# Optimization experiments

Measured on AMD Instinct MI355X. Metric: run time of the kernel, lower is better.

Reference implementation:

```python
import jax, jax.numpy as jnp
import numpy as np

EPS = 1e-4  # IRLS smoothing epsilon

def _corr(x, k):
    # x: [C,H,W], k: [kh,kw]; cross-correlation, 'same' output, replicate (clamp) boundary
    ph, pw = k.shape[0] // 2, k.shape[1] // 2
    xp = jnp.pad(x, ((0, 0), (ph, ph), (pw, pw)), mode='edge')
    out = jax.lax.conv_general_dilated(xp[:, None], k[None, None].astype(x.dtype), (1, 1), 'VALID', dimension_numbers=('NCHW', 'OIHW', 'NCHW'))
    return out[:, 0]

def _flip(k):
    return k[::-1, ::-1]

def _forward(blurred, kernel, reg_kernels, reg_kernel_weights, reg_target_kernels, reg_powers, num_irls_iter, num_cg_iter):
    n = reg_kernels.shape[0]
    w_kernel = jnp.ones_like(blurred)                       # data-term weights (ones, as in forward)
    w_reg = jnp.ones((n,) + blurred.shape, blurred.dtype)   # IRLS reg weights, start at 1
    lam = reg_kernel_weights ** 2                           # squared weights keep A PSD

    def R(x, ks):  # apply each reg kernel -> [N,C,H,W]
        return jax.vmap(lambda k: _corr(x, k))(ks)

    def RT(y, ks):  # adjoint: correlate with flipped kernels, y: [N,C,H,W]
        return jax.vmap(lambda yi, k: _corr(yi, _flip(k)))(y, ks)

    def A(x, w_reg):  # A = K^T W K + sum_n lam_n R_n^T W_n R_n
        data = _corr(w_kernel * _corr(x, kernel), _flip(kernel))
        reg = jnp.einsum('n,nchw->chw', lam, RT(w_reg * R(x, reg_kernels), reg_kernels))
        return data + reg

    Tb = R(blurred, reg_target_kernels)           # regularization targets T_n b
    KtWb = _corr(w_kernel * blurred, _flip(kernel))
    x0 = blurred
    for _ in range(num_irls_iter):
        # DeconvCGInit: rhs and initial residual/search direction
        rhs = KtWb + jnp.einsum('n,nchw->chw', lam, RT(w_reg * Tb, reg_kernels))
        x = x0
        r = rhs - A(x, w_reg)
        p = r
        # DeconvCGIter: standard CG updates
        for _ in range(num_cg_iter):
            Ap = A(p, w_reg)
            rr = jnp.sum(r * r)
            alpha = rr / jnp.sum(p * Ap)
            x = x + alpha * p
            r = r - alpha * Ap
            beta = jnp.sum(r * r) / rr
            p = r + beta * p
        x0 = x
        # DeconvCGWeight: IRLS reweighting w_n = p_n * (|R_n x - T_n b| + eps)^(p_n - 2)
        d = R(x0, reg_kernels) - Tb
        pw = reg_powers[:, None, None, None]
        w_reg = pw * jnp.power(jnp.abs(d) + EPS, pw - 2.0)
    return x0

def setup_inputs():
    key = jax.random.key(0)
    ks = jax.random.split(key, 6)
    C, H, W = 3, 1024, 1024
    NREG, RKS, BKS = 5, 5, 15
    blurred = jax.random.uniform(ks[0], (C, H, W), jnp.float32)
    kernel = jax.random.uniform(ks[1], (BKS, BKS), jnp.float32)
    kernel = kernel / jnp.sum(kernel)  # normalized blur kernel
    rk = 0.1 * jax.random.normal(ks[2], (NREG, RKS, RKS), jnp.float32)
    rk = rk.at[0, 2, 2].add(-2.0).at[0, 3, 2].add(1.0).at[0, 2, 3].add(1.0)  # gradient stencil init
    rkw = 0.1 * jax.random.normal(ks[3], (NREG,), jnp.float32)
    rkw = rkw.at[0].add(1.0)
    rtk = 0.1 * jax.random.normal(ks[4], (NREG, RKS, RKS), jnp.float32)
    rp = 1.0 + 0.02 * jax.random.normal(ks[5], (NREG,), jnp.float32)
    return {"blurred": blurred, "kernel": kernel, "reg_kernels": rk, "reg_kernel_weights": rkw, "reg_target_kernels": rtk, "reg_powers": rp, "num_irls_iter": 2, "num_cg_iter": 4}

def reference(blurred, kernel, reg_kernels, reg_kernel_weights, reg_target_kernels, reg_powers, num_irls_iter, num_cg_iter):
    return _forward(blurred, kernel, reg_kernels, reg_kernel_weights, reg_target_kernels, reg_powers, num_irls_iter, num_cg_iter)
```

## Files before the change

kernel.cpp:

```cpp
#include <hip/hip_runtime.h>
#include <math.h>

#define HH 1024
#define WW 1024
#define CHN 3
#define PLANE (HH*WW)
#define IMG (CHN*PLANE)
#define NREG 5
#define EPSV 1e-4f

#define OFF_WREG 0
#define OFF_KTWB (5*IMG)
#define OFF_T    (6*IMG)
#define OFF_R    (7*IMG)
#define OFF_P    (8*IMG)
#define OFF_AP   (9*IMG)
#define OFF_PART (10*IMG)
#define OFF_SCAL (10*IMG + 3072)

__global__ __launch_bounds__(256) void k_init(const float4* __restrict__ b,
                                              float4* __restrict__ x,
                                              float4* __restrict__ wreg) {
  const int stride = gridDim.x * 256;
  const float4 one = make_float4(1.f, 1.f, 1.f, 1.f);
  for (int i = blockIdx.x * 256 + threadIdx.x; i < NREG * IMG / 4; i += stride) {
    wreg[i] = one;
    if (i < IMG / 4) x[i] = b[i];
  }
}

template <bool FLIP>
__global__ __launch_bounds__(256) void k_corr15(const float* __restrict__ in,
                                                const float* __restrict__ k15,
                                                float* __restrict__ out) {
  __shared__ float tile[142 * 78];
  const int c = blockIdx.z;
  const int R0 = blockIdx.y * 128;
  const int C0 = blockIdx.x * 64;
  const float* inc = in + c * PLANE;
  for (int i = threadIdx.x; i < 142 * 78; i += 256) {
    int r = i / 78, col = i - r * 78;
    int gr = min(max(R0 - 7 + r, 0), HH - 1);
    int gc = min(max(C0 - 7 + col, 0), WW - 1);
    tile[i] = inc[gr * WW + gc];
  }
  __syncthreads();
  const int tx = threadIdx.x & 7;
  const int ty = threadIdx.x >> 3;
  const int oi = ty * 4, oj = tx * 8;
  float acc[4][8];
#pragma unroll
  for (int o = 0; o < 4; ++o)
#pragma unroll
    for (int q = 0; q < 8; ++q) acc[o][q] = 0.f;

#pragma unroll 1
  for (int rr = 0; rr < 18; ++rr) {
    float wv[22];
#pragma unroll
    for (int q = 0; q < 22; ++q) wv[q] = tile[(oi + rr) * 78 + oj + q];
#pragma unroll
    for (int o = 0; o < 4; ++o) {
      int a = rr - o;
      if (a >= 0 && a < 15) {
#pragma unroll
        for (int b = 0; b < 15; ++b) {
          float kv = FLIP ? k15[(14 - a) * 15 + (14 - b)] : k15[a * 15 + b];
#pragma unroll
          for (int q = 0; q < 8; ++q) acc[o][q] = fmaf(kv, wv[b + q], acc[o][q]);
        }
      }
    }
  }
  float* oc = out + c * PLANE + (R0 + oi) * WW + C0 + oj;
#pragma unroll
  for (int o = 0; o < 4; ++o) {
    float4* dst = (float4*)(oc + o * WW);
    dst[0] = make_float4(acc[o][0], acc[o][1], acc[o][2], acc[o][3]);
    dst[1] = make_float4(acc[o][4], acc[o][5], acc[o][6], acc[o][7]);
  }
}

__device__ __forceinline__ void blk_reduce2(float a, float b, float* scratch,
                                            float* o1, float* o2) {
#pragma unroll
  for (int off = 32; off > 0; off >>= 1) {
    a += __shfl_down(a, off, 64);
    b += __shfl_down(b, off, 64);
  }
  __syncthreads();
  const int lane = threadIdx.x & 63, wid = threadIdx.x >> 6;
  if (lane == 0) { scratch[wid] = a; scratch[4 + wid] = b; }
  __syncthreads();
  if (threadIdx.x == 0) {
    *o1 = scratch[0] + scratch[1] + scratch[2] + scratch[3];
    *o2 = scratch[4] + scratch[5] + scratch[6] + scratch[7];
  }
}

template <int MODE>
__global__ __launch_bounds__(256) void k_reg(
    const float* __restrict__ src, const float* __restrict__ tin,
    const float* __restrict__ k15, const float* __restrict__ rk,
    const float* __restrict__ kin_all, const float* __restrict__ rkw,
    const float* __restrict__ wreg, const float* __restrict__ ktwb,
    const float* __restrict__ apin, const float* __restrict__ rin,
    float* __restrict__ out, float* __restrict__ pout,
    float* __restrict__ part) {
  __shared__ float sbuf[78 * 78];
  __shared__ float vbuf[68 * 68];
  const int c = blockIdx.z;
  const int R0 = blockIdx.y * 64, C0 = blockIdx.x * 64;
  const int tid = threadIdx.x;

  const float* sc = src + c * PLANE;
  for (int i = tid; i < 72 * 72; i += 256) {
    int r = i / 72, col = i - r * 72;
    int gr = min(max(R0 - 4 + r, 0), HH - 1);
    int gc = min(max(C0 - 4 + col, 0), WW - 1);
    sbuf[r * 78 + col] = sc[gr * WW + gc];
  }
  __syncthreads();

  const int tx = tid & 15, ty = tid >> 4;
  const int oi = ty * 4, oj = tx * 4;
  float acc[4][4];
#pragma unroll
  for (int o = 0; o < 4; ++o)
#pragma unroll
    for (int q = 0; q < 4; ++q) acc[o][q] = 0.f;

#pragma unroll 1
  for (int n = 0; n < NREG; ++n) {
    float lw = rkw[n];
    const float lam = lw * lw;
    const float* kin = kin_all + n * 25;
    const float* kout = rk + n * 25;
    const float* wr = wreg + (n * CHN + c) * PLANE;
    for (int e = tid; e < 68 * 68; e += 256) {
      int vr = e / 68, vc = e - vr * 68;
      int cgr = min(max(R0 - 2 + vr, 0), HH - 1);
      int cgc = min(max(C0 - 2 + vc, 0), WW - 1);
      int sr = cgr - R0 + 2;
      int scl = cgc - C0 + 2;
      float s = 0.f;
#pragma unroll
      for (int a = 0; a < 5; ++a)
#pragma unroll
        for (int b = 0; b < 5; ++b)
          s = fmaf(kin[a * 5 + b], sbuf[(sr + a) * 78 + scl + b], s);
      vbuf[e] = s * wr[cgr * WW + cgc];
    }
    __syncthreads();
#pragma unroll 1
    for (int ra = 0; ra < 8; ++ra) {
      float vw[8];
#pragma unroll
      for (int q = 0; q < 8; ++q) vw[q] = vbuf[(oi + ra) * 68 + oj + q];
#pragma unroll
      for (int o = 0; o < 4; ++o) {
        int a = ra - o;
        if (a >= 0 && a < 5) {
#pragma unroll
          for (int b = 0; b < 5; ++b) {
            float kv = lam * kout[(4 - a) * 5 + (4 - b)];
#pragma unroll
            for (int q = 0; q < 4; ++q) acc[o][q] = fmaf(kv, vw[b + q], acc[o][q]);
          }
        }
      }
    }
    __syncthreads();
  }

  if constexpr (MODE != 2) {
    const float* tc = tin + c * PLANE;
    for (int i = tid; i < 78 * 78; i += 256) {
      int r = i / 78, col = i - r * 78;
      int gr = min(max(R0 - 7 + r, 0), HH - 1);
      int gc = min(max(C0 - 7 + col, 0), WW - 1);
      sbuf[i] = tc[gr * WW + gc];
    }
    __syncthreads();
#pragma unroll 1
    for (int rr = 0; rr < 18; ++rr) {
      float wv[19];
#pragma unroll
      for (int q = 0; q < 19; ++q) wv[q] = sbuf[(oi + rr) * 78 + oj + q];
#pragma unroll
      for (int o = 0; o < 4; ++o) {
        int a = rr - o;
        if (a >= 0 && a < 15) {
#pragma unroll
          for (int b = 0; b < 15; ++b) {
            float kv = k15[(14 - a) * 15 + (14 - b)];
#pragma unroll
            for (int q = 0; q < 4; ++q) acc[o][q] = fmaf(kv, wv[b + q], acc[o][q]);
          }
        }
      }
    }
  }

  const int obase = c * PLANE + (R0 + oi) * WW + C0 + oj;
  if constexpr (MODE != 2) {
#pragma unroll
    for (int o = 0; o < 4; ++o)
      *(float4*)(out + obase + o * WW) =
          make_float4(acc[o][0], acc[o][1], acc[o][2], acc[o][3]);
    if constexpr (MODE == 0) {
      float pap = 0.f, rr2 = 0.f;
#pragma unroll
      for (int o = 0; o < 4; ++o) {
        float4 pv = *(const float4*)(src + obase + o * WW);
        float4 rv = *(const float4*)(rin + obase + o * WW);
        pap += acc[o][0] * pv.x + acc[o][1] * pv.y + acc[o][2] * pv.z + acc[o][3] * pv.w;
        rr2 += rv.x * rv.x + rv.y * rv.y + rv.z * rv.z + rv.w * rv.w;
      }
      float s1, s2;
      blk_reduce2(pap, rr2, vbuf, &s1, &s2);
      if (tid == 0) {
        int bid = (blockIdx.z * 16 + blockIdx.y) * 16 + blockIdx.x;
        part[bid] = s1;
        part[1024 + bid] = s2;
      }
    }
  } else {
#pragma unroll
    for (int o = 0; o < 4; ++o) {
      float4 kw = *(const float4*)(ktwb + obase + o * WW);
      float4 ap = *(const float4*)(apin + obase + o * WW);
      float4 rv = make_float4(kw.x - ap.x + acc[o][0], kw.y - ap.y + acc[o][1],
                              kw.z - ap.z + acc[o][2], kw.w - ap.w + acc[o][3]);
      *(float4*)(out + obase + o * WW) = rv;
      *(float4*)(pout + obase + o * WW) = rv;
    }
  }
}

__global__ __launch_bounds__(256) void k_wupd(
    const float* __restrict__ x, const float* __restrict__ blur,
    const float* __restrict__ rk, const float* __restrict__ rtk,
    const float* __restrict__ rp, float* __restrict__ wreg) {
  __shared__ float xb[68 * 68];
  __shared__ float bb[68 * 68];
  const int c = blockIdx.z, R0 = blockIdx.y * 64, C0 = blockIdx.x * 64;
  const int tid = threadIdx.x;
  const float* xc = x + c * PLANE;
  const float* bc = blur + c * PLANE;
  for (int i = tid; i < 68 * 68; i += 256) {
    int r = i / 68, col = i - r * 68;
    int gr = min(max(R0 - 2 + r, 0), HH - 1);
    int gc = min(max(C0 - 2 + col, 0), WW - 1);
    xb[i] = xc[gr * WW + gc];
    bb[i] = bc[gr * WW + gc];
  }
  __syncthreads();
  const int tx = tid & 15, ty = tid >> 4;
  const int oi = ty * 4, oj = tx * 4;
#pragma unroll 1
  for (int n = 0; n < NREG; ++n) {
    const float* k1 = rk + n * 25;
    const float* k2 = rtk + n * 25;
    float pw = rp[n];
    float* wc = wreg + (n * CHN + c) * PLANE + (R0 + oi) * WW + C0 + oj;
#pragma unroll
    for (int o = 0; o < 4; ++o) {
      float tmp[4];
#pragma unroll
      for (int q = 0; q < 4; ++q) {
        float d = 0.f;
#pragma unroll
        for (int a = 0; a < 5; ++a)
#pragma unroll
          for (int b = 0; b < 5; ++b) {
            int idx = (oi + o + a) * 68 + oj + q + b;
            d += k1[a * 5 + b] * xb[idx] - k2[a * 5 + b] * bb[idx];
          }
        tmp[q] = pw * powf(fabsf(d) + EPSV, pw - 2.0f);
      }
      *(float4*)(wc + o * WW) = make_float4(tmp[0], tmp[1], tmp[2], tmp[3]);
    }
  }
}

__global__ __launch_bounds__(256) void k_sumfin1(const float* __restrict__ part,
                                                 float* __restrict__ scal) {
  __shared__ float scratch[8];
  float a = 0.f, b = 0.f;
  for (int i = threadIdx.x; i < 768; i += 256) {
    a += part[i];
    b += part[1024 + i];
  }
  float s1, s2;
  blk_reduce2(a, b, scratch, &s1, &s2);
  if (threadIdx.x == 0) {
    scal[0] = s2 / s1;
    scal[1] = s2;
  }
}

__global__ __launch_bounds__(256) void k_upd_xr(
    float4* __restrict__ x, const float4* __restrict__ p,
    float4* __restrict__ r, const float4* __restrict__ ap,
    const float* __restrict__ scal, float* __restrict__ part2) {
  __shared__ float scratch[8];
  const float alpha = scal[0];
  float s = 0.f;
  const int stride = gridDim.x * 256;
  for (int i = blockIdx.x * 256 + threadIdx.x; i < IMG / 4; i += stride) {
    float4 xv = x[i], pv = p[i], rv = r[i], av = ap[i];
    xv.x += alpha * pv.x; xv.y += alpha * pv.y; xv.z += alpha * pv.z; xv.w += alpha * pv.w;
    rv.x -= alpha * av.x; rv.y -= alpha * av.y; rv.z -= alpha * av.z; rv.w -= alpha * av.w;
    x[i] = xv; r[i] = rv;
    s += rv.x * rv.x + rv.y * rv.y + rv.z * rv.z + rv.w * rv.w;
  }
#pragma unroll
  for (int off = 32; off > 0; off >>= 1) s += __shfl_down(s, off, 64);
  if ((threadIdx.x & 63) == 0) scratch[threadIdx.x >> 6] = s;
  __syncthreads();
  if (threadIdx.x == 0)
    part2[blockIdx.x] = scratch[0] + scratch[1] + scratch[2] + scratch[3];
}

__global__ __launch_bounds__(256) void k_upd_x(
    float4* __restrict__ x, const float4* __restrict__ p,
    const float* __restrict__ scal) {
  const float alpha = scal[0];
  const int stride = gridDim.x * 256;
  for (int i = blockIdx.x * 256 + threadIdx.x; i < IMG / 4; i += stride) {
    float4 xv = x[i], pv = p[i];
    xv.x += alpha * pv.x; xv.y += alpha * pv.y; xv.z += alpha * pv.z; xv.w += alpha * pv.w;
    x[i] = xv;
  }
}

__global__ __launch_bounds__(256) void k_sumfin2(const float* __restrict__ part2,
                                                 float* __restrict__ scal) {
  __shared__ float scratch[8];
  float a = 0.f;
  for (int i = threadIdx.x; i < 768; i += 256) a += part2[i];
  float s1, s2;
  blk_reduce2(a, 0.f, scratch, &s1, &s2);
  if (threadIdx.x == 0) scal[2] = s1 / scal[1];
}

__global__ __launch_bounds__(256) void k_upd_p(
    float4* __restrict__ p, const float4* __restrict__ r,
    const float* __restrict__ scal) {
  const float beta = scal[2];
  const int stride = gridDim.x * 256;
  for (int i = blockIdx.x * 256 + threadIdx.x; i < IMG / 4; i += stride) {
    float4 pv = p[i], rv = r[i];
    pv.x = rv.x + beta * pv.x; pv.y = rv.y + beta * pv.y;
    pv.z = rv.z + beta * pv.z; pv.w = rv.w + beta * pv.w;
    p[i] = pv;
  }
}

extern "C" void kernel_launch(void* const* d_in, const int* in_sizes, int n_in,
                              void* d_out, int out_size, void* d_ws, size_t ws_size,
                              hipStream_t stream) {
  (void)in_sizes; (void)n_in; (void)out_size; (void)ws_size;
  const float* blurred = (const float*)d_in[0];
  const float* k15 = (const float*)d_in[1];
  const float* rk  = (const float*)d_in[2];
  const float* rkw = (const float*)d_in[3];
  const float* rtk = (const float*)d_in[4];
  const float* rp  = (const float*)d_in[5];

  float* x = (float*)d_out;
  float* ws = (float*)d_ws;
  float* wreg  = ws + OFF_WREG;
  float* ktwb  = ws + OFF_KTWB;
  float* t     = ws + OFF_T;
  float* r     = ws + OFF_R;
  float* p     = ws + OFF_P;
  float* ap    = ws + OFF_AP;
  float* part  = ws + OFF_PART;
  float* part2 = part + 2048;
  float* scal  = ws + OFF_SCAL;

  const dim3 b256(256);
  const dim3 g15(16, 8, CHN);
  const dim3 g64(16, 16, CHN);

  k_init<<<dim3(2048), b256, 0, stream>>>((const float4*)blurred, (float4*)x,
                                          (float4*)wreg);
  k_corr15<true><<<g15, b256, 0, stream>>>(blurred, k15, ktwb);

  for (int irls = 0; irls < 2; ++irls) {
    k_corr15<false><<<g15, b256, 0, stream>>>(x, k15, t);
    k_reg<1><<<g64, b256, 0, stream>>>(x, t, k15, rk, rk, rkw, wreg,
                                       nullptr, nullptr, nullptr, ap, nullptr, nullptr);
    k_reg<2><<<g64, b256, 0, stream>>>(blurred, nullptr, k15, rk, rtk, rkw, wreg,
                                       ktwb, ap, nullptr, r, p, nullptr);
    for (int cg = 0; cg < 4; ++cg) {
      const bool last = (cg == 3);
      k_corr15<false><<<g15, b256, 0, stream>>>(p, k15, t);
      k_reg<0><<<g64, b256, 0, stream>>>(p, t, k15, rk, rk, rkw, wreg,
                                         nullptr, nullptr, r, ap, nullptr, part);
      k_sumfin1<<<dim3(1), b256, 0, stream>>>(part, scal);
      if (!last) {
        k_upd_xr<<<dim3(768), b256, 0, stream>>>((float4*)x, (const float4*)p,
                                                 (float4*)r, (const float4*)ap,
                                                 scal, part2);
        k_sumfin2<<<dim3(1), b256, 0, stream>>>(part2, scal);
        k_upd_p<<<dim3(768), b256, 0, stream>>>((float4*)p, (const float4*)r, scal);
      } else {
        k_upd_x<<<dim3(768), b256, 0, stream>>>((float4*)x, (const float4*)p, scal);
      }
    }
    if (irls == 0)
      k_wupd<<<g64, b256, 0, stream>>>(x, blurred, rk, rtk, rp, wreg);
  }
}
```

Measured before the change: 1.727 ms.

## Restructure convolution kernels, split K^T pass out, fold scalar reductions into updates

The 15x15 correlation now uses 128-thread blocks on 64x72 tiles, reads the kernel as float4 from padded shared memory, and pads the tile row stride. The adjoint blur pass is taken out of k_reg and run as its own k_corr15 that writes into ap, which k_reg then accumulates into. k_reg and k_wupd are rewritten as column-per-lane 16-row sliding windows with kernels cached in shared memory and padded strides, and powf is replaced by __expf/__logf. The separate single-block sumfin kernels are removed by having every update block redo the small partial-sum reduction itself. This cuts launches and shared-memory bank conflicts, but adds an extra full-image pass through ap and uses lower-accuracy power math.

```diff
diff --git a/kernel.cpp b/kernel.cpp
--- a/kernel.cpp
+++ b/kernel.cpp
@@ -16,7 +16,6 @@
 #define OFF_P    (8*IMG)
 #define OFF_AP   (9*IMG)
 #define OFF_PART (10*IMG)
-#define OFF_SCAL (10*IMG + 3072)
 
 __global__ __launch_bounds__(256) void k_init(const float4* __restrict__ b,
                                               float4* __restrict__ x,
@@ -30,54 +29,67 @@
 }
 
 template <bool FLIP>
-__global__ __launch_bounds__(256) void k_corr15(const float* __restrict__ in,
+__global__ __launch_bounds__(128) void k_corr15(const float* __restrict__ in,
                                                 const float* __restrict__ k15,
                                                 float* __restrict__ out) {
-  __shared__ float tile[142 * 78];
-  const int c = blockIdx.z;
-  const int R0 = blockIdx.y * 128;
-  const int C0 = blockIdx.x * 64;
-  const float* inc = in + c * PLANE;
-  for (int i = threadIdx.x; i < 142 * 78; i += 256) {
-    int r = i / 78, col = i - r * 78;
+  __shared__ float tile[78 * 87];
+  __shared__ float kpad[15 * 16];
+  const int ch = blockIdx.z;
+  const int R0 = blockIdx.y * 64;
+  const int C0 = blockIdx.x * 72;
+  const int tid = threadIdx.x;
+  for (int i = tid; i < 240; i += 128) {
+    int a = i >> 4, b = i & 15;
+    float v = 0.f;
+    if (b < 15) v = FLIP ? k15[(14 - a) * 15 + (14 - b)] : k15[a * 15 + b];
+    kpad[i] = v;
+  }
+  const float* inc = in + ch * PLANE;
+  for (int i = tid; i < 78 * 86; i += 128) {
+    int r = i / 86, c = i - r * 86;
     int gr = min(max(R0 - 7 + r, 0), HH - 1);
-    int gc = min(max(C0 - 7 + col, 0), WW - 1);
-    tile[i] = inc[gr * WW + gc];
-  }
-  __syncthreads();
-  const int tx = threadIdx.x & 7;
-  const int ty = threadIdx.x >> 3;
-  const int oi = ty * 4, oj = tx * 8;
-  float acc[4][8];
+    int gc = min(max(C0 - 7 + c, 0), WW - 1);
+    tile[r * 87 + c] = inc[gr * WW + gc];
+  }
+  __syncthreads();
+  const int tx = tid & 7, ty = tid >> 3;
+  const int oi = ty * 4, oj = tx * 9;
+  float acc[4][9];
 #pragma unroll
   for (int o = 0; o < 4; ++o)
 #pragma unroll
-    for (int q = 0; q < 8; ++q) acc[o][q] = 0.f;
+    for (int q = 0; q < 9; ++q) acc[o][q] = 0.f;
 
 #pragma unroll 1
   for (int rr = 0; rr < 18; ++rr) {
-    float wv[22];
-#pragma unroll
-    for (int q = 0; q < 22; ++q) wv[q] = tile[(oi + rr) * 78 + oj + q];
+    float wv[23];
+#pragma unroll
+    for (int q = 0; q < 23; ++q) wv[q] = tile[(oi + rr) * 87 + oj + q];
 #pragma unroll
     for (int o = 0; o < 4; ++o) {
       int a = rr - o;
-      if (a >= 0 && a < 15) {
-#pragma unroll
-        for (int b = 0; b < 15; ++b) {
-          float kv = FLIP ? k15[(14 - a) * 15 + (14 - b)] : k15[a * 15 + b];
-#pragma unroll
-          for (int q = 0; q < 8; ++q) acc[o][q] = fmaf(kv, wv[b + q], acc[o][q]);
-        }
-      }
-    }
-  }
-  float* oc = out + c * PLANE + (R0 + oi) * WW + C0 + oj;
+      if ((unsigned)a < 15u) {
+        const float4* kp = (const float4*)&kpad[a * 16];
+        float4 kA = kp[0], kB = kp[1], kC = kp[2], kD = kp[3];
+        float kv[16] = {kA.x, kA.y, kA.z, kA.w, kB.x, kB.y, kB.z, kB.w,
+                        kC.x, kC.y, kC.z, kC.w, kD.x, kD.y, kD.z, kD.w};
+#pragma unroll
+        for (int b = 0; b < 15; ++b)
+#pragma unroll
+          for (int q = 0; q < 9; ++q)
+            acc[o][q] = fmaf(kv[b], wv[b + q], acc[o][q]);
+      }
+    }
+  }
+  float* oc = out + ch * PLANE;
 #pragma unroll
   for (int o = 0; o < 4; ++o) {
-    float4* dst = (float4*)(oc + o * WW);
-    dst[0] = make_float4(acc[o][0], acc[o][1], acc[o][2], acc[o][3]);
-    dst[1] = make_float4(acc[o][4], acc[o][5], acc[o][6], acc[o][7]);
+    const int orow = R0 + oi + o;
+#pragma unroll
+    for (int q = 0; q < 9; ++q) {
+      int gcol = C0 + oj + q;
+      if (gcol < WW) oc[orow * WW + gcol] = acc[o][q];
+    }
   }
 }
 
@@ -100,141 +112,138 @@
 
 template <int MODE>
 __global__ __launch_bounds__(256) void k_reg(
-    const float* __restrict__ src, const float* __restrict__ tin,
-    const float* __restrict__ k15, const float* __restrict__ rk,
-    const float* __restrict__ kin_all, const float* __restrict__ rkw,
+    const float* __restrict__ src, const float* __restrict__ kin_all,
+    const float* __restrict__ rk, const float* __restrict__ rkw,
     const float* __restrict__ wreg, const float* __restrict__ ktwb,
-    const float* __restrict__ apin, const float* __restrict__ rin,
-    float* __restrict__ out, float* __restrict__ pout,
+    float* __restrict__ ap, const float* __restrict__ rin,
+    float* __restrict__ rout, float* __restrict__ pout,
     float* __restrict__ part) {
-  __shared__ float sbuf[78 * 78];
-  __shared__ float vbuf[68 * 68];
-  const int c = blockIdx.z;
+  __shared__ float sbuf[72 * 73];
+  __shared__ float vbuf[68 * 69];
+  __shared__ float kin_s[NREG * 25];
+  __shared__ float kf_s[NREG * 25];
+  __shared__ float scratch[8];
+  const int ch = blockIdx.z;
   const int R0 = blockIdx.y * 64, C0 = blockIdx.x * 64;
   const int tid = threadIdx.x;
-
-  const float* sc = src + c * PLANE;
+  const int lane = tid & 63, wid = tid >> 6;
+  const int W = wid * 16;
+
+  if (tid < NREG * 25) {
+    int n = tid / 25, j = tid - n * 25, a = j / 5, b = j - a * 5;
+    kin_s[tid] = kin_all[tid];
+    float lw = rkw[n];
+    kf_s[tid] = lw * lw * rk[n * 25 + (4 - a) * 5 + (4 - b)];
+  }
+  const float* sc = src + ch * PLANE;
   for (int i = tid; i < 72 * 72; i += 256) {
-    int r = i / 72, col = i - r * 72;
+    int r = i / 72, c = i - r * 72;
     int gr = min(max(R0 - 4 + r, 0), HH - 1);
-    int gc = min(max(C0 - 4 + col, 0), WW - 1);
-    sbuf[r * 78 + col] = sc[gr * WW + gc];
-  }
-  __syncthreads();
-
-  const int tx = tid & 15, ty = tid >> 4;
-  const int oi = ty * 4, oj = tx * 4;
-  float acc[4][4];
-#pragma unroll
-  for (int o = 0; o < 4; ++o)
-#pragma unroll
-    for (int q = 0; q < 4; ++q) acc[o][q] = 0.f;
-
-#pragma unroll 1
+    int gc = min(max(C0 - 4 + c, 0), WW - 1);
+    sbuf[r * 73 + c] = sc[gr * WW + gc];
+  }
+  __syncthreads();
+
+  float acc[16];
+#pragma unroll
+  for (int s = 0; s < 16; ++s) acc[s] = 0.f;
+
   for (int n = 0; n < NREG; ++n) {
-    float lw = rkw[n];
-    const float lam = lw * lw;
-    const float* kin = kin_all + n * 25;
-    const float* kout = rk + n * 25;
-    const float* wr = wreg + (n * CHN + c) * PLANE;
-    for (int e = tid; e < 68 * 68; e += 256) {
-      int vr = e / 68, vc = e - vr * 68;
-      int cgr = min(max(R0 - 2 + vr, 0), HH - 1);
-      int cgc = min(max(C0 - 2 + vc, 0), WW - 1);
-      int sr = cgr - R0 + 2;
-      int scl = cgc - C0 + 2;
+    float kin[25];
+#pragma unroll
+    for (int j = 0; j < 25; ++j) kin[j] = kin_s[n * 25 + j];
+    const float* wn = wreg + (n * CHN + ch) * PLANE;
+
+    for (int e = tid; e < 528; e += 256) {
+      int vr, vc;
+      if (e < 136)      { vr = e / 68;                 vc = e - (e / 68) * 68; }
+      else if (e < 272) { int j2 = e - 136; vr = 66 + j2 / 68; vc = j2 - (j2 / 68) * 68; }
+      else if (e < 400) { int j2 = e - 272; vr = 2 + (j2 >> 1); vc = j2 & 1; }
+      else              { int j2 = e - 400; vr = 2 + (j2 >> 1); vc = 66 + (j2 & 1); }
+      int rc = min(max(R0 - 2 + vr, 0), HH - 1);
+      int cc = min(max(C0 - 2 + vc, 0), WW - 1);
+      int tr = rc - R0 + 2, tc = cc - C0 + 2;
       float s = 0.f;
 #pragma unroll
       for (int a = 0; a < 5; ++a)
 #pragma unroll
         for (int b = 0; b < 5; ++b)
-          s = fmaf(kin[a * 5 + b], sbuf[(sr + a) * 78 + scl + b], s);
-      vbuf[e] = s * wr[cgr * WW + cgc];
-    }
+          s = fmaf(kin[a * 5 + b], sbuf[(tr + a) * 73 + tc + b], s);
+      vbuf[vr * 69 + vc] = s * wn[rc * WW + cc];
+    }
+
+    float vacc[16];
+#pragma unroll
+    for (int s = 0; s < 16; ++s) vacc[s] = 0.f;
+#pragma unroll
+    for (int rr = 0; rr < 20; ++rr) {
+      float x5[5];
+#pragma unroll
+      for (int b = 0; b < 5; ++b) x5[b] = sbuf[(W + 2 + rr) * 73 + lane + 2 + b];
+#pragma unroll
+      for (int a = 0; a < 5; ++a) {
+        int s = rr - a;
+        if (s >= 0 && s < 16) {
+#pragma unroll
+          for (int b = 0; b < 5; ++b) vacc[s] = fmaf(kin[a * 5 + b], x5[b], vacc[s]);
+        }
+      }
+    }
+#pragma unroll
+    for (int s = 0; s < 16; ++s)
+      vbuf[(2 + W + s) * 69 + lane + 2] = vacc[s] * wn[(R0 + W + s) * WW + C0 + lane];
     __syncthreads();
-#pragma unroll 1
-    for (int ra = 0; ra < 8; ++ra) {
-      float vw[8];
-#pragma unroll
-      for (int q = 0; q < 8; ++q) vw[q] = vbuf[(oi + ra) * 68 + oj + q];
-#pragma unroll
-      for (int o = 0; o < 4; ++o) {
-        int a = ra - o;
-        if (a >= 0 && a < 5) {
-#pragma unroll
-          for (int b = 0; b < 5; ++b) {
-            float kv = lam * kout[(4 - a) * 5 + (4 - b)];
-#pragma unroll
-            for (int q = 0; q < 4; ++q) acc[o][q] = fmaf(kv, vw[b + q], acc[o][q]);
-          }
+
+    float kf[25];
+#pragma unroll
+    for (int j = 0; j < 25; ++j) kf[j] = kf_s[n * 25 + j];
+#pragma unroll
+    for (int rv = 0; rv < 20; ++rv) {
+      float v5[5];
+#pragma unroll
+      for (int b = 0; b < 5; ++b) v5[b] = vbuf[(W + rv) * 69 + lane + b];
+#pragma unroll
+      for (int a = 0; a < 5; ++a) {
+        int s = rv - a;
+        if (s >= 0 && s < 16) {
+#pragma unroll
+          for (int b = 0; b < 5; ++b) acc[s] = fmaf(kf[a * 5 + b], v5[b], acc[s]);
         }
       }
     }
     __syncthreads();
   }
 
-  if constexpr (MODE != 2) {
-    const float* tc = tin + c * PLANE;
-    for (int i = tid; i < 78 * 78; i += 256) {
-      int r = i / 78, col = i - r * 78;
-      int gr = min(max(R0 - 7 + r, 0), HH - 1);
-      int gc = min(max(C0 - 7 + col, 0), WW - 1);
-      sbuf[i] = tc[gr * WW + gc];
-    }
-    __syncthreads();
-#pragma unroll 1
-    for (int rr = 0; rr < 18; ++rr) {
-      float wv[19];
-#pragma unroll
-      for (int q = 0; q < 19; ++q) wv[q] = sbuf[(oi + rr) * 78 + oj + q];
-#pragma unroll
-      for (int o = 0; o < 4; ++o) {
-        int a = rr - o;
-        if (a >= 0 && a < 15) {
-#pragma unroll
-          for (int b = 0; b < 15; ++b) {
-            float kv = k15[(14 - a) * 15 + (14 - b)];
-#pragma unroll
-            for (int q = 0; q < 4; ++q) acc[o][q] = fmaf(kv, wv[b + q], acc[o][q]);
-          }
-        }
-      }
-    }
-  }
-
-  const int obase = c * PLANE + (R0 + oi) * WW + C0 + oj;
-  if constexpr (MODE != 2) {
-#pragma unroll
-    for (int o = 0; o < 4; ++o)
-      *(float4*)(out + obase + o * WW) =
-          make_float4(acc[o][0], acc[o][1], acc[o][2], acc[o][3]);
+  const int obase = ch * PLANE + (R0 + W) * WW + C0 + lane;
+  if constexpr (MODE == 2) {
+#pragma unroll
+    for (int s = 0; s < 16; ++s) {
+      float rv = ktwb[obase + s * WW] - ap[obase + s * WW] + acc[s];
+      rout[obase + s * WW] = rv;
+      pout[obase + s * WW] = rv;
+    }
+  } else {
+    float pap = 0.f, rr2 = 0.f;
+#pragma unroll
+    for (int s = 0; s < 16; ++s) {
+      float av = ap[obase + s * WW] + acc[s];
+      ap[obase + s * WW] = av;
+      if constexpr (MODE == 0) {
+        float pv = src[obase + s * WW];
+        float rv = rin[obase + s * WW];
+        pap = fmaf(av, pv, pap);
+        rr2 = fmaf(rv, rv, rr2);
+      }
+    }
     if constexpr (MODE == 0) {
-      float pap = 0.f, rr2 = 0.f;
-#pragma unroll
-      for (int o = 0; o < 4; ++o) {
-        float4 pv = *(const float4*)(src + obase + o * WW);
-        float4 rv = *(const float4*)(rin + obase + o * WW);
-        pap += acc[o][0] * pv.x + acc[o][1] * pv.y + acc[o][2] * pv.z + acc[o][3] * pv.w;
-        rr2 += rv.x * rv.x + rv.y * rv.y + rv.z * rv.z + rv.w * rv.w;
-      }
       float s1, s2;
-      blk_reduce2(pap, rr2, vbuf, &s1, &s2);
+      blk_reduce2(pap, rr2, scratch, &s1, &s2);
       if (tid == 0) {
         int bid = (blockIdx.z * 16 + blockIdx.y) * 16 + blockIdx.x;
         part[bid] = s1;
         part[1024 + bid] = s2;
       }
     }
-  } else {
-#pragma unroll
-    for (int o = 0; o < 4; ++o) {
-      float4 kw = *(const float4*)(ktwb + obase + o * WW);
-      float4 ap = *(const float4*)(apin + obase + o * WW);
-      float4 rv = make_float4(kw.x - ap.x + acc[o][0], kw.y - ap.y + acc[o][1],
-                              kw.z - ap.z + acc[o][2], kw.w - ap.w + acc[o][3]);
-      *(float4*)(out + obase + o * WW) = rv;
-      *(float4*)(pout + obase + o * WW) = rv;
-    }
   }
 }
 
@@ -242,70 +251,80 @@
     const float* __restrict__ x, const float* __restrict__ blur,
     const float* __restrict__ rk, const float* __restrict__ rtk,
     const float* __restrict__ rp, float* __restrict__ wreg) {
-  __shared__ float xb[68 * 68];
-  __shared__ float bb[68 * 68];
-  const int c = blockIdx.z, R0 = blockIdx.y * 64, C0 = blockIdx.x * 64;
+  __shared__ float xb[68 * 69];
+  __shared__ float bb[68 * 69];
+  __shared__ float k1s[NREG * 25], k2s[NREG * 25];
+  __shared__ float rps[NREG];
+  const int ch = blockIdx.z, R0 = blockIdx.y * 64, C0 = blockIdx.x * 64;
   const int tid = threadIdx.x;
-  const float* xc = x + c * PLANE;
-  const float* bc = blur + c * PLANE;
+  const int lane = tid & 63, wid = tid >> 6, W = wid * 16;
+  if (tid < NREG * 25) { k1s[tid] = rk[tid]; k2s[tid] = rtk[tid]; }
+  if (tid < NREG) rps[tid] = rp[tid];
+  const float* xc = x + ch * PLANE;
+  const float* bc = blur + ch * PLANE;
   for (int i = tid; i < 68 * 68; i += 256) {
-    int r = i / 68, col = i - r * 68;
+    int r = i / 68, c = i - r * 68;
     int gr = min(max(R0 - 2 + r, 0), HH - 1);
-    int gc = min(max(C0 - 2 + col, 0), WW - 1);
-    xb[i] = xc[gr * WW + gc];
-    bb[i] = bc[gr * WW + gc];
-  }
-  __syncthreads();
-  const int tx = tid & 15, ty = tid >> 4;
-  const int oi = ty * 4, oj = tx * 4;
-#pragma unroll 1
+    int gc = min(max(C0 - 2 + c, 0), WW - 1);
+    xb[r * 69 + c] = xc[gr * WW + gc];
+    bb[r * 69 + c] = bc[gr * WW + gc];
+  }
+  __syncthreads();
   for (int n = 0; n < NREG; ++n) {
-    const float* k1 = rk + n * 25;
-    const float* k2 = rtk + n * 25;
-    float pw = rp[n];
-    float* wc = wreg + (n * CHN + c) * PLANE + (R0 + oi) * WW + C0 + oj;
-#pragma unroll
-    for (int o = 0; o < 4; ++o) {
-      float tmp[4];
-#pragma unroll
-      for (int q = 0; q < 4; ++q) {
-        float d = 0.f;
-#pragma unroll
-        for (int a = 0; a < 5; ++a)
+    float k1[25], k2[25];
+#pragma unroll
+    for (int j = 0; j < 25; ++j) { k1[j] = k1s[n * 25 + j]; k2[j] = k2s[n * 25 + j]; }
+    float d_[16];
+#pragma unroll
+    for (int s = 0; s < 16; ++s) d_[s] = 0.f;
+#pragma unroll
+    for (int rr = 0; rr < 20; ++rr) {
+      float x5[5], b5[5];
+#pragma unroll
+      for (int b = 0; b < 5; ++b) {
+        x5[b] = xb[(W + rr) * 69 + lane + b];
+        b5[b] = bb[(W + rr) * 69 + lane + b];
+      }
+#pragma unroll
+      for (int a = 0; a < 5; ++a) {
+        int s = rr - a;
+        if (s >= 0 && s < 16) {
 #pragma unroll
           for (int b = 0; b < 5; ++b) {
-            int idx = (oi + o + a) * 68 + oj + q + b;
-            d += k1[a * 5 + b] * xb[idx] - k2[a * 5 + b] * bb[idx];
+            d_[s] = fmaf(k1[a * 5 + b], x5[b], d_[s]);
+            d_[s] = fmaf(-k2[a * 5 + b], b5[b], d_[s]);
           }
-        tmp[q] = pw * powf(fabsf(d) + EPSV, pw - 2.0f);
-      }
-      *(float4*)(wc + o * WW) = make_float4(tmp[0], tmp[1], tmp[2], tmp[3]);
-    }
-  }
-}
-
-__global__ __launch_bounds__(256) void k_sumfin1(const float* __restrict__ part,
-                                                 float* __restrict__ scal) {
-  __shared__ float scratch[8];
-  float a = 0.f, b = 0.f;
-  for (int i = threadIdx.x; i < 768; i += 256) {
-    a += part[i];
-    b += part[1024 + i];
-  }
-  float s1, s2;
-  blk_reduce2(a, b, scratch, &s1, &s2);
-  if (threadIdx.x == 0) {
-    scal[0] = s2 / s1;
-    scal[1] = s2;
+        }
+      }
+    }
+    float pw = rps[n];
+    float* wc = wreg + (n * CHN + ch) * PLANE + (R0 + W) * WW + C0 + lane;
+#pragma unroll
+    for (int s = 0; s < 16; ++s) {
+      float v = fabsf(d_[s]) + EPSV;
+      wc[s * WW] = pw * __expf((pw - 2.f) * __logf(v));
+    }
   }
 }
 
 __global__ __launch_bounds__(256) void k_upd_xr(
     float4* __restrict__ x, const float4* __restrict__ p,
     float4* __restrict__ r, const float4* __restrict__ ap,
-    const float* __restrict__ scal, float* __restrict__ part2) {
+    const float* __restrict__ part, float* __restrict__ part2) {
   __shared__ float scratch[8];
-  const float alpha = scal[0];
+  __shared__ float sAlpha;
+  {
+    float a = 0.f, b = 0.f;
+    for (int i = threadIdx.x; i < 768; i += 256) {
+      a += part[i];
+      b += part[1024 + i];
+    }
+    float s1, s2;
+    blk_reduce2(a, b, scratch, &s1, &s2);
+    if (threadIdx.x == 0) sAlpha = s2 / s1;
+    __syncthreads();
+  }
+  const float alpha = sAlpha;
   float s = 0.f;
   const int stride = gridDim.x * 256;
   for (int i = blockIdx.x * 256 + threadIdx.x; i < IMG / 4; i += stride) {
@@ -317,6 +336,7 @@
   }
 #pragma unroll
   for (int off = 32; off > 0; off >>= 1) s += __shfl_down(s, off, 64);
+  __syncthreads();
   if ((threadIdx.x & 63) == 0) scratch[threadIdx.x >> 6] = s;
   __syncthreads();
   if (threadIdx.x == 0)
@@ -325,8 +345,21 @@
 
 __global__ __launch_bounds__(256) void k_upd_x(
     float4* __restrict__ x, const float4* __restrict__ p,
-    const float* __restrict__ scal) {
-  const float alpha = scal[0];
+    const float* __restrict__ part) {
+  __shared__ float scratch[8];
+  __shared__ float sAlpha;
+  {
+    float a = 0.f, b = 0.f;
+    for (int i = threadIdx.x; i < 768; i += 256) {
+      a += part[i];
+      b += part[1024 + i];
+    }
+    float s1, s2;
+    blk_reduce2(a, b, scratch, &s1, &s2);
+    if (threadIdx.x == 0) sAlpha = s2 / s1;
+    __syncthreads();
+  }
+  const float alpha = sAlpha;
   const int stride = gridDim.x * 256;
   for (int i = blockIdx.x * 256 + threadIdx.x; i < IMG / 4; i += stride) {
     float4 xv = x[i], pv = p[i];
@@ -335,20 +368,23 @@
   }
 }
 
-__global__ __launch_bounds__(256) void k_sumfin2(const float* __restrict__ part2,
-                                                 float* __restrict__ scal) {
-  __shared__ float scratch[8];
-  float a = 0.f;
-  for (int i = threadIdx.x; i < 768; i += 256) a += part2[i];
-  float s1, s2;
-  blk_reduce2(a, 0.f, scratch, &s1, &s2);
-  if (threadIdx.x == 0) scal[2] = s1 / scal[1];
-}
-
 __global__ __launch_bounds__(256) void k_upd_p(
     float4* __restrict__ p, const float4* __restrict__ r,
-    const float* __restrict__ scal) {
-  const float beta = scal[2];
+    const float* __restrict__ part, const float* __restrict__ part2) {
+  __shared__ float scratch[8];
+  __shared__ float sBeta;
+  {
+    float a = 0.f, b = 0.f;
+    for (int i = threadIdx.x; i < 768; i += 256) {
+      a += part2[i];
+      b += part[1024 + i];
+    }
+    float s1, s2;
+    blk_reduce2(a, b, scratch, &s1, &s2);
+    if (threadIdx.x == 0) sBeta = s1 / s2;
+    __syncthreads();
+  }
+  const float beta = sBeta;
   const int stride = gridDim.x * 256;
   for (int i = blockIdx.x * 256 + threadIdx.x; i < IMG / 4; i += stride) {
     float4 pv = p[i], rv = r[i];
@@ -379,36 +415,36 @@
   float* ap    = ws + OFF_AP;
   float* part  = ws + OFF_PART;
   float* part2 = part + 2048;
-  float* scal  = ws + OFF_SCAL;
-
-  const dim3 b256(256);
-  const dim3 g15(16, 8, CHN);
+
+  const dim3 b256(256), b128(128);
+  const dim3 g15(15, 16, CHN);
   const dim3 g64(16, 16, CHN);
 
   k_init<<<dim3(2048), b256, 0, stream>>>((const float4*)blurred, (float4*)x,
                                           (float4*)wreg);
-  k_corr15<true><<<g15, b256, 0, stream>>>(blurred, k15, ktwb);
+  k_corr15<true><<<g15, b128, 0, stream>>>(blurred, k15, ktwb);
 
   for (int irls = 0; irls < 2; ++irls) {
-    k_corr15<false><<<g15, b256, 0, stream>>>(x, k15, t);
-    k_reg<1><<<g64, b256, 0, stream>>>(x, t, k15, rk, rk, rkw, wreg,
-                                       nullptr, nullptr, nullptr, ap, nullptr, nullptr);
-    k_reg<2><<<g64, b256, 0, stream>>>(blurred, nullptr, k15, rk, rtk, rkw, wreg,
-                                       ktwb, ap, nullptr, r, p, nullptr);
+    k_corr15<false><<<g15, b128, 0, stream>>>(x, k15, t);
+    k_corr15<true><<<g15, b128, 0, stream>>>(t, k15, ap);
+    k_reg<1><<<g64, b256, 0, stream>>>(x, rk, rk, rkw, wreg, nullptr, ap,
+                                       nullptr, nullptr, nullptr, nullptr);
+    k_reg<2><<<g64, b256, 0, stream>>>(blurred, rtk, rk, rkw, wreg, ktwb, ap,
+                                       nullptr, r, p, nullptr);
     for (int cg = 0; cg < 4; ++cg) {
       const bool last = (cg == 3);
-      k_corr15<false><<<g15, b256, 0, stream>>>(p, k15, t);
-      k_reg<0><<<g64, b256, 0, stream>>>(p, t, k15, rk, rk, rkw, wreg,
-                                         nullptr, nullptr, r, ap, nullptr, part);
-      k_sumfin1<<<dim3(1), b256, 0, stream>>>(part, scal);
+      k_corr15<false><<<g15, b128, 0, stream>>>(p, k15, t);
+      k_corr15<true><<<g15, b128, 0, stream>>>(t, k15, ap);
+      k_reg<0><<<g64, b256, 0, stream>>>(p, rk, rk, rkw, wreg, nullptr, ap,
+                                         r, nullptr, nullptr, part);
       if (!last) {
         k_upd_xr<<<dim3(768), b256, 0, stream>>>((float4*)x, (const float4*)p,
                                                  (float4*)r, (const float4*)ap,
-                                                 scal, part2);
-        k_sumfin2<<<dim3(1), b256, 0, stream>>>(part2, scal);
-        k_upd_p<<<dim3(768), b256, 0, stream>>>((float4*)p, (const float4*)r, scal);
+                                                 part, part2);
+        k_upd_p<<<dim3(768), b256, 0, stream>>>((float4*)p, (const float4*)r,
+                                                part, part2);
       } else {
-        k_upd_x<<<dim3(768), b256, 0, stream>>>((float4*)x, (const float4*)p, scal);
+        k_upd_x<<<dim3(768), b256, 0, stream>>>((float4*)x, (const float4*)p, part);
       }
     }
     if (irls == 0)
```

Result: faster. 1.654 ms (-4.2%).
